# Kernel tuning notes

Hardware: AMD Instinct MI355X
Metric: run time of the kernel (lower is better)

The kernel has to match this reference:

```python
import jax, jax.numpy as jnp
import numpy as np

N = 50000
NEG_SLOPE = 0.2

def gat_conv(x, src, dst, W, a_src, a_dst, bias, heads, out_ch):
    # Linear projection per head: [N, H, C]
    h = (x @ W).reshape(x.shape[0], heads, out_ch)
    # Node-level attention terms alpha_src/alpha_dst: [N, H]
    al_src = jnp.einsum('nhc,hc->nh', h, a_src)
    al_dst = jnp.einsum('nhc,hc->nh', h, a_dst)
    # Edge logits with LeakyReLU: [E, H]
    logits = jax.nn.leaky_relu(al_src[src] + al_dst[dst], NEG_SLOPE)
    # Segment softmax over incoming edges of each dst node
    m = jax.ops.segment_max(logits, dst, num_segments=N)
    e = jnp.exp(logits - m[dst])
    s = jax.ops.segment_sum(e, dst, num_segments=N)
    alpha = e / (s[dst] + 1e-16)                      # [E, H]
    # Weighted message aggregation (scatter-add): [N, H, C]
    out = jax.ops.segment_sum(h[src] * alpha[..., None], dst, num_segments=N)
    return out.reshape(N, heads * out_ch) + bias


def setup_inputs() -> dict:
    key = jax.random.key(0)
    ks = jax.random.split(key, 12)
    in_ch, out_ch = 128, 256
    h1, c1 = 4, out_ch // 8          # conv1: 4 heads x 32
    mid = h1 * c1                    # 128 = out_ch // 2
    E = 1600000
    x = jax.random.normal(ks[0], (N, in_ch), jnp.float32)
    edge_index = jax.random.randint(ks[1], (2, E), 0, N, jnp.int64)
    sc = 0.1
    return {
        'x': x,
        'edge_index': edge_index,
        'W1': jax.random.normal(ks[2], (in_ch, h1 * c1), jnp.float32) * sc,
        'a_src1': jax.random.normal(ks[3], (h1, c1), jnp.float32) * sc,
        'a_dst1': jax.random.normal(ks[4], (h1, c1), jnp.float32) * sc,
        'b1': jnp.zeros((h1 * c1,), jnp.float32),
        'W2': jax.random.normal(ks[5], (mid, out_ch), jnp.float32) * sc,
        'a_src2': jax.random.normal(ks[6], (1, out_ch), jnp.float32) * sc,
        'a_dst2': jax.random.normal(ks[7], (1, out_ch), jnp.float32) * sc,
        'b2': jnp.zeros((out_ch,), jnp.float32),
    }


def reference(x, edge_index, W1, a_src1, a_dst1, b1, W2, a_src2, a_dst2, b2):
    # PyG GATConv adds self-loops by default
    loop = jnp.arange(N, dtype=edge_index.dtype)
    src = jnp.concatenate([edge_index[0], loop])
    dst = jnp.concatenate([edge_index[1], loop])
    h = gat_conv(x, src, dst, W1, a_src1, a_dst1, b1, heads=4, out_ch=32)
    h = jax.nn.relu(h)
    out = gat_conv(h, src, dst, W2, a_src2, a_dst2, b2, heads=1, out_ch=256)
    return out
```

## Files before the change

### kernel.cpp

```cpp
#include <hip/hip_runtime.h>
#include <hip/hip_fp16.h>
#include <math.h>

#define NSLOPE 0.2f

typedef _Float16 half8 __attribute__((ext_vector_type(8)));
typedef float floatx4 __attribute__((ext_vector_type(4)));

__device__ __forceinline__ float lrelu(float t) { return t > 0.f ? t : NSLOPE * t; }

__device__ __forceinline__ void fma8h(float* acc, float w, const uint4& v) {
    const __half2* h2 = reinterpret_cast<const __half2*>(&v);
#pragma unroll
    for (int i = 0; i < 4; ++i) {
        float2 f = __half22float2(h2[i]);
        acc[2 * i]     = fmaf(w, f.x, acc[2 * i]);
        acc[2 * i + 1] = fmaf(w, f.y, acc[2 * i + 1]);
    }
}

#define MAXB 5632
#define BE   8192

__global__ __launch_bounds__(256)
void bucketA_kernel(const int* __restrict__ src, const int* __restrict__ dst,
                    int* __restrict__ bcnt, int E, int Etot, int nb)
{
    __shared__ int hist[512];
    int tid = threadIdx.x;
    for (int i = tid; i < 512; i += 256) hist[i] = 0;
    __syncthreads();
    for (int e = blockIdx.x * 256 + tid; e < Etot; e += gridDim.x * 256) {
        int d = (e < E) ? dst[e] : (e - E);
        atomicAdd(&hist[d >> 7], 1);
    }
    __syncthreads();
    for (int i = tid; i < nb; i += 256) {
        int v = hist[i];
        if (v) atomicAdd(&bcnt[i], v);
    }
}

__global__ __launch_bounds__(512)
void scanBuckets_kernel(const int* __restrict__ bcnt, int* __restrict__ bbase,
                        int* __restrict__ gcur, int nb, int* __restrict__ offs,
                        int N, int total)
{
    __shared__ int tmp[512];
    int tid = threadIdx.x;
    int v = (tid < nb) ? bcnt[tid] : 0;
    tmp[tid] = v;
    __syncthreads();
    for (int off = 1; off < 512; off <<= 1) {
        int t = (tid >= off) ? tmp[tid - off] : 0;
        __syncthreads();
        tmp[tid] += t;
        __syncthreads();
    }
    if (tid < nb) {
        int e = tmp[tid] - v;
        bbase[tid] = e;
        gcur[tid] = e;
    }
    if (tid == 0) offs[N] = total;
}

__global__ __launch_bounds__(256)
void bucketB_kernel(const int* __restrict__ src, const int* __restrict__ dst,
                    int* __restrict__ gcur, unsigned* __restrict__ eout,
                    int E, int Etot, int nb)
{
    __shared__ int hist[512];
    __shared__ int res[512];
    __shared__ int lcur[512];
    int tid = threadIdx.x;
    int e0 = blockIdx.x * BE;
    int e1 = min(e0 + BE, Etot);

    for (int i = tid; i < 512; i += 256) hist[i] = 0;
    __syncthreads();
    for (int e = e0 + tid; e < e1; e += 256) {
        int d = (e < E) ? dst[e] : (e - E);
        atomicAdd(&hist[d >> 7], 1);
    }
    __syncthreads();
    for (int i = tid; i < nb; i += 256) {
        int h = hist[i];
        res[i] = h ? atomicAdd(&gcur[i], h) : 0;
        lcur[i] = 0;
    }
    __syncthreads();
    for (int e = e0 + tid; e < e1; e += 256) {
        int s, d;
        if (e < E) { s = src[e]; d = dst[e]; }
        else       { s = e - E; d = s; }
        int b = d >> 7;
        int p = res[b] + atomicAdd(&lcur[b], 1);
        eout[p] = (unsigned)s | ((unsigned)(d & 127) << 16);
    }
}

__global__ __launch_bounds__(256)
void bucketC_kernel(const unsigned* __restrict__ eout, const int* __restrict__ bbase,
                    const int* __restrict__ bcnt, unsigned short* __restrict__ csr,
                    int* __restrict__ offs, int N)
{
    __shared__ unsigned eb[MAXB];
    __shared__ unsigned short sbuf[MAXB];
    __shared__ int cnt128[128], cur128[128], sc[128];

    int b = blockIdx.x;
    int tid = threadIdx.x;
    int ebase = bbase[b];
    int ecnt = bcnt[b];
    int n0 = b << 7;
    int ncount = min(128, N - n0);

    if (tid < 128) cnt128[tid] = 0;
    for (int i = tid; i < ecnt; i += 256) eb[i] = eout[ebase + i];
    __syncthreads();
    for (int i = tid; i < ecnt; i += 256) atomicAdd(&cnt128[eb[i] >> 16], 1);
    __syncthreads();
    if (tid < 128) sc[tid] = cnt128[tid];
    __syncthreads();
    for (int off = 1; off < 128; off <<= 1) {
        int t = (tid >= off && tid < 128) ? sc[tid - off] : 0;
        __syncthreads();
        if (tid < 128) sc[tid] += t;
        __syncthreads();
    }
    if (tid < 128) {
        int excl = sc[tid] - cnt128[tid];
        cur128[tid] = excl;
        if (tid < ncount) offs[n0 + tid] = ebase + excl;
    }
    __syncthreads();
    for (int i = tid; i < ecnt; i += 256) {
        unsigned v = eb[i];
        int p = atomicAdd(&cur128[v >> 16], 1);
        sbuf[p] = (unsigned short)(v & 0xFFFFu);
    }
    __syncthreads();
    for (int i = tid; i < ecnt; i += 256) csr[ebase + i] = sbuf[i];
}

__global__ __launch_bounds__(256)
void w2sd_kernel(const float* __restrict__ W2, const float* __restrict__ a_src2,
                 const float* __restrict__ a_dst2, float* __restrict__ w2s,
                 float* __restrict__ w2d)
{
    int t = threadIdx.x;
    const float* a = (t < 128) ? a_src2 : a_dst2;
    int k = t & 127;
    float acc = 0.f;
    for (int c = 0; c < 256; c += 4) {
        float4 w = *(const float4*)&W2[(size_t)k * 256 + c];
        float4 av = *(const float4*)&a[c];
        acc = fmaf(w.x, av.x, fmaf(w.y, av.y, fmaf(w.z, av.z, fmaf(w.w, av.w, acc))));
    }
    if (t < 128) w2s[k] = acc; else w2d[k] = acc;
}

__global__ __launch_bounds__(256)
void cast_f2h_kernel(const float* __restrict__ in, __half* __restrict__ out, int n)
{
    int i = (blockIdx.x * 256 + threadIdx.x) * 4;
    if (i >= n) return;
    float4 v = *(const float4*)&in[i];
    __half2 a = __floats2half2_rn(v.x, v.y);
    __half2 b = __floats2half2_rn(v.z, v.w);
    *(uint2*)&out[i] = make_uint2(*(unsigned*)&a, *(unsigned*)&b);
}

__global__ __launch_bounds__(128)
void transposeW_kernel(const float* __restrict__ W, __half* __restrict__ WT, int C)
{
    int c = blockIdx.x;
    int k = threadIdx.x;
    WT[(size_t)c * 128 + k] = __float2half(W[(size_t)k * C + c]);
}

__global__ __launch_bounds__(256)
void gemm1_mfma(const __half* __restrict__ A16, const __half* __restrict__ W1T,
                const float* __restrict__ a_src, const float* __restrict__ a_dst,
                __half* __restrict__ h1, float* __restrict__ al_src,
                float* __restrict__ al_dst, int M)
{
    int wave = threadIdx.x >> 6, lane = threadIdx.x & 63;
    int lr = lane & 15, q = lane >> 4;
    int r0 = blockIdx.x * 32 + (wave >> 1) * 16;
    int wcol = (wave & 1) * 64;

    int arow = min(r0 + lr, M - 1);
    const uint4* Arow = (const uint4*)A16 + (size_t)arow * 16;
    half8 a[4];
#pragma unroll
    for (int kb = 0; kb < 4; ++kb) {
        union { uint4 u; half8 h; } c;
        c.u = Arow[kb * 4 + q];
        a[kb] = c.h;
    }

    floatx4 acc[4];
    const floatx4 zero = {0.f, 0.f, 0.f, 0.f};
#pragma unroll
    for (int ct = 0; ct < 4; ++ct) acc[ct] = zero;

#pragma unroll
    for (int ct = 0; ct < 4; ++ct) {
        const uint4* Brow = (const uint4*)W1T + (size_t)(wcol + ct * 16 + lr) * 16;
#pragma unroll
        for (int kb = 0; kb < 4; ++kb) {
            union { uint4 u; half8 h; } c;
            c.u = Brow[kb * 4 + q];
            acc[ct] = __builtin_amdgcn_mfma_f32_16x16x32_f16(a[kb], c.h, acc[ct], 0, 0, 0);
        }
    }

#pragma unroll
    for (int ct = 0; ct < 4; ++ct) {
        int col = wcol + ct * 16 + lr;
#pragma unroll
        for (int r = 0; r < 4; ++r) {
            int row = r0 + q * 4 + r;
            if (row < M) h1[(size_t)row * 128 + col] = __float2half(acc[ct][r]);
        }
    }

    float as[4], ad[4];
#pragma unroll
    for (int ct = 0; ct < 4; ++ct) {
        int col = wcol + ct * 16 + lr;
        as[ct] = a_src[col];
        ad[ct] = a_dst[col];
    }
    int hb = wcol >> 5;
#pragma unroll
    for (int r = 0; r < 4; ++r) {
        float psA = acc[0][r] * as[0] + acc[1][r] * as[1];
        float psB = acc[2][r] * as[2] + acc[3][r] * as[3];
        float pdA = acc[0][r] * ad[0] + acc[1][r] * ad[1];
        float pdB = acc[2][r] * ad[2] + acc[3][r] * ad[3];
#pragma unroll
        for (int off = 1; off < 16; off <<= 1) {
            psA += __shfl_xor(psA, off); psB += __shfl_xor(psB, off);
            pdA += __shfl_xor(pdA, off); pdB += __shfl_xor(pdB, off);
        }
        if (lr == 0) {
            int row = r0 + q * 4 + r;
            if (row < M) {
                al_src[(size_t)row * 4 + hb]     = psA;
                al_src[(size_t)row * 4 + hb + 1] = psB;
                al_dst[(size_t)row * 4 + hb]     = pdA;
                al_dst[(size_t)row * 4 + hb + 1] = pdB;
            }
        }
    }
}

__global__ __launch_bounds__(256)
void gemm2_mfma(const __half* __restrict__ A16, const __half* __restrict__ W2T,
                const float* __restrict__ bias, float* __restrict__ out, int M)
{
    int wave = threadIdx.x >> 6, lane = threadIdx.x & 63;
    int lr = lane & 15, q = lane >> 4;
    int r0 = blockIdx.x * 16;
    int c0 = wave * 64;

    int arow = min(r0 + lr, M - 1);
    const uint4* Arow = (const uint4*)A16 + (size_t)arow * 16;
    half8 a[4];
#pragma unroll
    for (int kb = 0; kb < 4; ++kb) {
        union { uint4 u; half8 h; } c;
        c.u = Arow[kb * 4 + q];
        a[kb] = c.h;
    }

    floatx4 acc[4];
    const floatx4 zero = {0.f, 0.f, 0.f, 0.f};
#pragma unroll
    for (int ct = 0; ct < 4; ++ct) acc[ct] = zero;

#pragma unroll
    for (int ct = 0; ct < 4; ++ct) {
        const uint4* Brow = (const uint4*)W2T + (size_t)(c0 + ct * 16 + lr) * 16;
#pragma unroll
        for (int kb = 0; kb < 4; ++kb) {
            union { uint4 u; half8 h; } c;
            c.u = Brow[kb * 4 + q];
            acc[ct] = __builtin_amdgcn_mfma_f32_16x16x32_f16(a[kb], c.h, acc[ct], 0, 0, 0);
        }
    }

#pragma unroll
    for (int ct = 0; ct < 4; ++ct) {
        int col = c0 + ct * 16 + lr;
        float b = bias[col];
#pragma unroll
        for (int r = 0; r < 4; ++r) {
            int row = r0 + q * 4 + r;
            if (row < M) out[(size_t)row * 256 + col] = acc[ct][r] + b;
        }
    }
}

__global__ __launch_bounds__(256)
void agg1_kernel(const __half* __restrict__ feat, const unsigned short* __restrict__ csr_src,
                 const int* __restrict__ offs, const float* __restrict__ alS,
                 const float* __restrict__ alD, const float* __restrict__ bias,
                 const float* __restrict__ w2s, const float* __restrict__ w2d,
                 __half* __restrict__ hmid, float* __restrict__ alS2,
                 float* __restrict__ alD2, int N)
{
    int lane = threadIdx.x & 63;
    int n = blockIdx.x * 4 + (threadIdx.x >> 6);
    if (n >= N) return;

    int lc = lane & 15;
    int es = lane >> 4;
    int h = lc >> 2;

    float aD = alD[(size_t)n * 4 + h];
    int beg = offs[n], end = offs[n + 1];

    float acc0[8] = {0,0,0,0,0,0,0,0}, acc1[8] = {0,0,0,0,0,0,0,0};
    float sw0 = 0.f, sw1 = 0.f;
    const uint4* feat16 = (const uint4*)feat;

    int j = beg + es;
    for (; j + 4 < end; j += 8) {
        int s0 = csr_src[j];
        int s1 = csr_src[j + 4];
        float w0 = __expf(lrelu(alS[(size_t)s0 * 4 + h] + aD));
        float w1 = __expf(lrelu(alS[(size_t)s1 * 4 + h] + aD));
        uint4 f0 = feat16[(size_t)s0 * 16 + lc];
        uint4 f1 = feat16[(size_t)s1 * 16 + lc];
        fma8h(acc0, w0, f0); sw0 += w0;
        fma8h(acc1, w1, f1); sw1 += w1;
    }
    if (j < end) {
        int s0 = csr_src[j];
        float w0 = __expf(lrelu(alS[(size_t)s0 * 4 + h] + aD));
        uint4 f0 = feat16[(size_t)s0 * 16 + lc];
        fma8h(acc0, w0, f0); sw0 += w0;
    }

    float sw = sw0 + sw1;
    sw += __shfl_xor(sw, 16); sw += __shfl_xor(sw, 32);
#pragma unroll
    for (int i = 0; i < 8; ++i) {
        acc0[i] += acc1[i];
        acc0[i] += __shfl_xor(acc0[i], 16);
        acc0[i] += __shfl_xor(acc0[i], 32);
    }

    if (lane < 16) {
        float inv = 1.f / (sw + 1e-16f);
        float v[8];
#pragma unroll
        for (int i = 0; i < 8; ++i)
            v[i] = fmaxf(fmaf(acc0[i], inv, bias[lc * 8 + i]), 0.f);
        __half2 p0 = __floats2half2_rn(v[0], v[1]);
        __half2 p1 = __floats2half2_rn(v[2], v[3]);
        __half2 p2 = __floats2half2_rn(v[4], v[5]);
        __half2 p3 = __floats2half2_rn(v[6], v[7]);
        uint4 pk = make_uint4(*(unsigned*)&p0, *(unsigned*)&p1,
                              *(unsigned*)&p2, *(unsigned*)&p3);
        ((uint4*)hmid)[(size_t)n * 16 + lc] = pk;
        float ps = 0.f, pd = 0.f;
#pragma unroll
        for (int i = 0; i < 8; ++i) {
            ps = fmaf(v[i], w2s[lc * 8 + i], ps);
            pd = fmaf(v[i], w2d[lc * 8 + i], pd);
        }
        ps += __shfl_xor(ps, 1); ps += __shfl_xor(ps, 2);
        ps += __shfl_xor(ps, 4); ps += __shfl_xor(ps, 8);
        pd += __shfl_xor(pd, 1); pd += __shfl_xor(pd, 2);
        pd += __shfl_xor(pd, 4); pd += __shfl_xor(pd, 8);
        if (lane == 0) { alS2[n] = ps; alD2[n] = pd; }
    }
}

__global__ __launch_bounds__(256)
void agg2_kernel(const __half* __restrict__ feat, const unsigned short* __restrict__ csr_src,
                 const int* __restrict__ offs, const float* __restrict__ alS,
                 const float* __restrict__ alD, __half* __restrict__ m16, int N)
{
    int lane = threadIdx.x & 63;
    int n = blockIdx.x * 4 + (threadIdx.x >> 6);
    if (n >= N) return;

    int lc = lane & 15;
    int es = lane >> 4;

    float aD = alD[n];
    int beg = offs[n], end = offs[n + 1];

    float acc0[8] = {0,0,0,0,0,0,0,0}, acc1[8] = {0,0,0,0,0,0,0,0};
    float sw0 = 0.f, sw1 = 0.f;
    const uint4* feat16 = (const uint4*)feat;

    int j = beg + es;
    for (; j + 4 < end; j += 8) {
        int s0 = csr_src[j];
        int s1 = csr_src[j + 4];
        float w0 = __expf(lrelu(alS[s0] + aD));
        float w1 = __expf(lrelu(alS[s1] + aD));
        uint4 f0 = feat16[(size_t)s0 * 16 + lc];
        uint4 f1 = feat16[(size_t)s1 * 16 + lc];
        fma8h(acc0, w0, f0); sw0 += w0;
        fma8h(acc1, w1, f1); sw1 += w1;
    }
    if (j < end) {
        int s0 = csr_src[j];
        float w0 = __expf(lrelu(alS[s0] + aD));
        uint4 f0 = feat16[(size_t)s0 * 16 + lc];
        fma8h(acc0, w0, f0); sw0 += w0;
    }

    float sw = sw0 + sw1;
    sw += __shfl_xor(sw, 16); sw += __shfl_xor(sw, 32);
#pragma unroll
    for (int i = 0; i < 8; ++i) {
        acc0[i] += acc1[i];
        acc0[i] += __shfl_xor(acc0[i], 16);
        acc0[i] += __shfl_xor(acc0[i], 32);
    }

    if (lane < 16) {
        float inv = 1.f / (sw + 1e-16f);
        float v[8];
#pragma unroll
        for (int i = 0; i < 8; ++i) v[i] = acc0[i] * inv;
        __half2 p0 = __floats2half2_rn(v[0], v[1]);
        __half2 p1 = __floats2half2_rn(v[2], v[3]);
        __half2 p2 = __floats2half2_rn(v[4], v[5]);
        __half2 p3 = __floats2half2_rn(v[6], v[7]);
        uint4 pk = make_uint4(*(unsigned*)&p0, *(unsigned*)&p1,
                              *(unsigned*)&p2, *(unsigned*)&p3);
        ((uint4*)m16)[(size_t)n * 16 + lc] = pk;
    }
}

extern "C" void kernel_launch(void* const* d_in, const int* in_sizes, int n_in,
                              void* d_out, int out_size, void* d_ws, size_t ws_size,
                              hipStream_t stream)
{
    const float* x      = (const float*)d_in[0];
    const int*   ei     = (const int*)d_in[1];
    const float* W1     = (const float*)d_in[2];
    const float* a_src1 = (const float*)d_in[3];
    const float* a_dst1 = (const float*)d_in[4];
    const float* b1     = (const float*)d_in[5];
    const float* W2     = (const float*)d_in[6];
    const float* a_src2 = (const float*)d_in[7];
    const float* a_dst2 = (const float*)d_in[8];
    const float* b2     = (const float*)d_in[9];

    const int N    = in_sizes[0] / 128;
    const int E    = in_sizes[1] / 2;
    const int Etot = E + N;
    const int* src = ei;
    const int* dst = ei + E;
    const int nb   = (N + 127) >> 7;

    char* ws = (char*)d_ws;
    size_t off = 0;
    auto carve = [&](size_t bytes) -> void* {
        void* p = ws + off;
        off += (bytes + 255) & ~(size_t)255;
        return p;
    };
    __half*  x16  = (__half*)carve((size_t)N * 128 * 2);
    __half*  h1   = (__half*)carve((size_t)N * 128 * 2);
    __half*  hmid = (__half*)carve((size_t)N * 128 * 2);
    __half*  m16  = (__half*)carve((size_t)N * 128 * 2);
    __half*  W1T  = (__half*)carve(128 * 128 * 2);
    __half*  W2T  = (__half*)carve(256 * 128 * 2);
    float*   alS1 = (float*)carve((size_t)N * 4 * 4);
    float*   alD1 = (float*)carve((size_t)N * 4 * 4);
    float*   alS2 = (float*)carve((size_t)N * 4);
    float*   alD2 = (float*)carve((size_t)N * 4);
    float*   w2s  = (float*)carve(128 * 4);
    float*   w2d  = (float*)carve(128 * 4);
    int*     offs = (int*)carve((size_t)(N + 1) * 4);
    int*     bcnt = (int*)carve(512 * 4);
    int*     bbas = (int*)carve(512 * 4);
    int*     gcur = (int*)carve(512 * 4);
    unsigned* eout = (unsigned*)carve((size_t)Etot * 4);
    unsigned short* csr = (unsigned short*)carve((size_t)Etot * 2);
    (void)ws_size; (void)n_in; (void)out_size;

    const int TB = 256;
    const int agrid = (N + 3) / 4;
    const int g1grid = (N + 31) / 32;
    const int g2grid = (N + 15) / 16;
    const int nx = N * 128;

    hipMemsetAsync(bcnt, 0, 512 * 4, stream);

    bucketA_kernel<<<512, TB, 0, stream>>>(src, dst, bcnt, E, Etot, nb);
    scanBuckets_kernel<<<1, 512, 0, stream>>>(bcnt, bbas, gcur, nb, offs, N, Etot);
    bucketB_kernel<<<(Etot + BE - 1) / BE, TB, 0, stream>>>(src, dst, gcur, eout, E, Etot, nb);
    bucketC_kernel<<<nb, TB, 0, stream>>>(eout, bbas, bcnt, csr, offs, N);

    cast_f2h_kernel<<<(nx / 4 + TB - 1) / TB, TB, 0, stream>>>(x, x16, nx);
    transposeW_kernel<<<128, 128, 0, stream>>>(W1, W1T, 128);
    transposeW_kernel<<<256, 128, 0, stream>>>(W2, W2T, 256);
    w2sd_kernel<<<1, 256, 0, stream>>>(W2, a_src2, a_dst2, w2s, w2d);

    gemm1_mfma<<<g1grid, 256, 0, stream>>>(x16, W1T, a_src1, a_dst1, h1, alS1, alD1, N);
    agg1_kernel<<<agrid, 256, 0, stream>>>(h1, csr, offs, alS1, alD1, b1,
                                           w2s, w2d, hmid, alS2, alD2, N);

    agg2_kernel<<<agrid, 256, 0, stream>>>(hmid, csr, offs, alS2, alD2, m16, N);
    gemm2_mfma<<<g2grid, 256, 0, stream>>>(m16, W2T, b2, (float*)d_out, N);
}
```

Before: 330.8 us.

## Merge independent prep kernels and co-schedule CSR bucketing with first GEMM

Folds bucket histogramming, the x cast, both weight transposes and the w2s/w2d projection into one block-partitioned prep kernel. It also merges the CSR bucketC pass with gemm1 into one combo kernel, so these independent stages share a launch and overlap on the GPU. This cuts launch count and idle tails between small kernels. In exchange, the combo kernel carries the large shared-memory footprint of the bucketing path into the GEMM blocks, which may lower their occupancy. The aggregation kernels also switch to byte-offset addressing for feature gathers, a minor address-arithmetic tweak.

```diff
diff --git a/kernel.cpp b/kernel.cpp
--- a/kernel.cpp
+++ b/kernel.cpp
@@ -23,21 +23,67 @@
 #define BE   8192
 
 __global__ __launch_bounds__(256)
-void bucketA_kernel(const int* __restrict__ src, const int* __restrict__ dst,
-                    int* __restrict__ bcnt, int E, int Etot, int nb)
+void prep_kernel(const int* __restrict__ dst, int* __restrict__ bcnt,
+                 const float* __restrict__ x, __half* __restrict__ x16, int nx,
+                 const float* __restrict__ W1, __half* __restrict__ W1T,
+                 const float* __restrict__ W2, __half* __restrict__ W2T,
+                 const float* __restrict__ a_src2, const float* __restrict__ a_dst2,
+                 float* __restrict__ w2s, float* __restrict__ w2d,
+                 int E, int Etot, int nb, int nbA, int ncast, int nt1, int nt2)
 {
     __shared__ int hist[512];
+    int bid = blockIdx.x;
     int tid = threadIdx.x;
-    for (int i = tid; i < 512; i += 256) hist[i] = 0;
-    __syncthreads();
-    for (int e = blockIdx.x * 256 + tid; e < Etot; e += gridDim.x * 256) {
-        int d = (e < E) ? dst[e] : (e - E);
-        atomicAdd(&hist[d >> 7], 1);
-    }
-    __syncthreads();
-    for (int i = tid; i < nb; i += 256) {
-        int v = hist[i];
-        if (v) atomicAdd(&bcnt[i], v);
+
+    if (bid < nbA) {
+        for (int i = tid; i < 512; i += 256) hist[i] = 0;
+        __syncthreads();
+        for (int e = bid * 256 + tid; e < Etot; e += nbA * 256) {
+            int d = (e < E) ? dst[e] : (e - E);
+            atomicAdd(&hist[d >> 7], 1);
+        }
+        __syncthreads();
+        for (int i = tid; i < nb; i += 256) {
+            int v = hist[i];
+            if (v) atomicAdd(&bcnt[i], v);
+        }
+        return;
+    }
+    bid -= nbA;
+    if (bid < ncast) {
+        int i = (bid * 256 + tid) * 4;
+        if (i < nx) {
+            float4 v = *(const float4*)&x[i];
+            __half2 a = __floats2half2_rn(v.x, v.y);
+            __half2 b = __floats2half2_rn(v.z, v.w);
+            *(uint2*)&x16[i] = make_uint2(*(unsigned*)&a, *(unsigned*)&b);
+        }
+        return;
+    }
+    bid -= ncast;
+    if (bid < nt1) {
+        int idx = bid * 256 + tid;
+        int c = idx >> 7, k = idx & 127;
+        W1T[(size_t)c * 128 + k] = __float2half(W1[(size_t)k * 128 + c]);
+        return;
+    }
+    bid -= nt1;
+    if (bid < nt2) {
+        int idx = bid * 256 + tid;
+        int c = idx >> 7, k = idx & 127;
+        W2T[(size_t)c * 128 + k] = __float2half(W2[(size_t)k * 256 + c]);
+        return;
+    }
+    {
+        const float* a = (tid < 128) ? a_src2 : a_dst2;
+        int k = tid & 127;
+        float acc = 0.f;
+        for (int c = 0; c < 256; c += 4) {
+            float4 w = *(const float4*)&W2[(size_t)k * 256 + c];
+            float4 av = *(const float4*)&a[c];
+            acc = fmaf(w.x, av.x, fmaf(w.y, av.y, fmaf(w.z, av.z, fmaf(w.w, av.w, acc))));
+        }
+        if (tid < 128) w2s[k] = acc; else w2d[k] = acc;
     }
 }
 
@@ -101,94 +147,60 @@
 }
 
 __global__ __launch_bounds__(256)
-void bucketC_kernel(const unsigned* __restrict__ eout, const int* __restrict__ bbase,
-                    const int* __restrict__ bcnt, unsigned short* __restrict__ csr,
-                    int* __restrict__ offs, int N)
+void combo_kernel(const unsigned* __restrict__ eout, const int* __restrict__ bbase,
+                  const int* __restrict__ bcnt, unsigned short* __restrict__ csr,
+                  int* __restrict__ offs, int N, int nb,
+                  const __half* __restrict__ A16, const __half* __restrict__ W1T,
+                  const float* __restrict__ a_src, const float* __restrict__ a_dst,
+                  __half* __restrict__ h1, float* __restrict__ al_src,
+                  float* __restrict__ al_dst)
 {
     __shared__ unsigned eb[MAXB];
     __shared__ unsigned short sbuf[MAXB];
     __shared__ int cnt128[128], cur128[128], sc[128];
 
-    int b = blockIdx.x;
     int tid = threadIdx.x;
-    int ebase = bbase[b];
-    int ecnt = bcnt[b];
-    int n0 = b << 7;
-    int ncount = min(128, N - n0);
-
-    if (tid < 128) cnt128[tid] = 0;
-    for (int i = tid; i < ecnt; i += 256) eb[i] = eout[ebase + i];
-    __syncthreads();
-    for (int i = tid; i < ecnt; i += 256) atomicAdd(&cnt128[eb[i] >> 16], 1);
-    __syncthreads();
-    if (tid < 128) sc[tid] = cnt128[tid];
-    __syncthreads();
-    for (int off = 1; off < 128; off <<= 1) {
-        int t = (tid >= off && tid < 128) ? sc[tid - off] : 0;
-        __syncthreads();
-        if (tid < 128) sc[tid] += t;
-        __syncthreads();
-    }
-    if (tid < 128) {
-        int excl = sc[tid] - cnt128[tid];
-        cur128[tid] = excl;
-        if (tid < ncount) offs[n0 + tid] = ebase + excl;
-    }
-    __syncthreads();
-    for (int i = tid; i < ecnt; i += 256) {
-        unsigned v = eb[i];
-        int p = atomicAdd(&cur128[v >> 16], 1);
-        sbuf[p] = (unsigned short)(v & 0xFFFFu);
-    }
-    __syncthreads();
-    for (int i = tid; i < ecnt; i += 256) csr[ebase + i] = sbuf[i];
-}
-
-__global__ __launch_bounds__(256)
-void w2sd_kernel(const float* __restrict__ W2, const float* __restrict__ a_src2,
-                 const float* __restrict__ a_dst2, float* __restrict__ w2s,
-                 float* __restrict__ w2d)
-{
-    int t = threadIdx.x;
-    const float* a = (t < 128) ? a_src2 : a_dst2;
-    int k = t & 127;
-    float acc = 0.f;
-    for (int c = 0; c < 256; c += 4) {
-        float4 w = *(const float4*)&W2[(size_t)k * 256 + c];
-        float4 av = *(const float4*)&a[c];
-        acc = fmaf(w.x, av.x, fmaf(w.y, av.y, fmaf(w.z, av.z, fmaf(w.w, av.w, acc))));
-    }
-    if (t < 128) w2s[k] = acc; else w2d[k] = acc;
-}
-
-__global__ __launch_bounds__(256)
-void cast_f2h_kernel(const float* __restrict__ in, __half* __restrict__ out, int n)
-{
-    int i = (blockIdx.x * 256 + threadIdx.x) * 4;
-    if (i >= n) return;
-    float4 v = *(const float4*)&in[i];
-    __half2 a = __floats2half2_rn(v.x, v.y);
-    __half2 b = __floats2half2_rn(v.z, v.w);
-    *(uint2*)&out[i] = make_uint2(*(unsigned*)&a, *(unsigned*)&b);
-}
-
-__global__ __launch_bounds__(128)
-void transposeW_kernel(const float* __restrict__ W, __half* __restrict__ WT, int C)
-{
-    int c = blockIdx.x;
-    int k = threadIdx.x;
-    WT[(size_t)c * 128 + k] = __float2half(W[(size_t)k * C + c]);
-}
-
-__global__ __launch_bounds__(256)
-void gemm1_mfma(const __half* __restrict__ A16, const __half* __restrict__ W1T,
-                const float* __restrict__ a_src, const float* __restrict__ a_dst,
-                __half* __restrict__ h1, float* __restrict__ al_src,
-                float* __restrict__ al_dst, int M)
-{
-    int wave = threadIdx.x >> 6, lane = threadIdx.x & 63;
+    if ((int)blockIdx.x < nb) {
+        int b = blockIdx.x;
+        int ebase = bbase[b];
+        int ecnt = bcnt[b];
+        int n0 = b << 7;
+        int ncount = min(128, N - n0);
+
+        if (tid < 128) cnt128[tid] = 0;
+        for (int i = tid; i < ecnt; i += 256) eb[i] = eout[ebase + i];
+        __syncthreads();
+        for (int i = tid; i < ecnt; i += 256) atomicAdd(&cnt128[eb[i] >> 16], 1);
+        __syncthreads();
+        if (tid < 128) sc[tid] = cnt128[tid];
+        __syncthreads();
+        for (int off = 1; off < 128; off <<= 1) {
+            int t = (tid >= off && tid < 128) ? sc[tid - off] : 0;
+            __syncthreads();
+            if (tid < 128) sc[tid] += t;
+            __syncthreads();
+        }
+        if (tid < 128) {
+            int excl = sc[tid] - cnt128[tid];
+            cur128[tid] = excl;
+            if (tid < ncount) offs[n0 + tid] = ebase + excl;
+        }
+        __syncthreads();
+        for (int i = tid; i < ecnt; i += 256) {
+            unsigned v = eb[i];
+            int p = atomicAdd(&cur128[v >> 16], 1);
+            sbuf[p] = (unsigned short)(v & 0xFFFFu);
+        }
+        __syncthreads();
+        for (int i = tid; i < ecnt; i += 256) csr[ebase + i] = sbuf[i];
+        return;
+    }
+
+    int gb = blockIdx.x - nb;
+    int M = N;
+    int wave = tid >> 6, lane = tid & 63;
     int lr = lane & 15, q = lane >> 4;
-    int r0 = blockIdx.x * 32 + (wave >> 1) * 16;
+    int r0 = gb * 32 + (wave >> 1) * 16;
     int wcol = (wave & 1) * 64;
 
     int arow = min(r0 + lr, M - 1);
@@ -326,7 +338,7 @@
 
     float acc0[8] = {0,0,0,0,0,0,0,0}, acc1[8] = {0,0,0,0,0,0,0,0};
     float sw0 = 0.f, sw1 = 0.f;
-    const uint4* feat16 = (const uint4*)feat;
+    const char* fbase = (const char*)feat + lc * 16;
 
     int j = beg + es;
     for (; j + 4 < end; j += 8) {
@@ -334,15 +346,15 @@
         int s1 = csr_src[j + 4];
         float w0 = __expf(lrelu(alS[(size_t)s0 * 4 + h] + aD));
         float w1 = __expf(lrelu(alS[(size_t)s1 * 4 + h] + aD));
-        uint4 f0 = feat16[(size_t)s0 * 16 + lc];
-        uint4 f1 = feat16[(size_t)s1 * 16 + lc];
+        uint4 f0 = *(const uint4*)(fbase + (size_t)s0 * 256);
+        uint4 f1 = *(const uint4*)(fbase + (size_t)s1 * 256);
         fma8h(acc0, w0, f0); sw0 += w0;
         fma8h(acc1, w1, f1); sw1 += w1;
     }
     if (j < end) {
         int s0 = csr_src[j];
         float w0 = __expf(lrelu(alS[(size_t)s0 * 4 + h] + aD));
-        uint4 f0 = feat16[(size_t)s0 * 16 + lc];
+        uint4 f0 = *(const uint4*)(fbase + (size_t)s0 * 256);
         fma8h(acc0, w0, f0); sw0 += w0;
     }
 
@@ -399,7 +411,7 @@
 
     float acc0[8] = {0,0,0,0,0,0,0,0}, acc1[8] = {0,0,0,0,0,0,0,0};
     float sw0 = 0.f, sw1 = 0.f;
-    const uint4* feat16 = (const uint4*)feat;
+    const char* fbase = (const char*)feat + lc * 16;
 
     int j = beg + es;
     for (; j + 4 < end; j += 8) {
@@ -407,15 +419,15 @@
         int s1 = csr_src[j + 4];
         float w0 = __expf(lrelu(alS[s0] + aD));
         float w1 = __expf(lrelu(alS[s1] + aD));
-        uint4 f0 = feat16[(size_t)s0 * 16 + lc];
-        uint4 f1 = feat16[(size_t)s1 * 16 + lc];
+        uint4 f0 = *(const uint4*)(fbase + (size_t)s0 * 256);
+        uint4 f1 = *(const uint4*)(fbase + (size_t)s1 * 256);
         fma8h(acc0, w0, f0); sw0 += w0;
         fma8h(acc1, w1, f1); sw1 += w1;
     }
     if (j < end) {
         int s0 = csr_src[j];
         float w0 = __expf(lrelu(alS[s0] + aD));
-        uint4 f0 = feat16[(size_t)s0 * 16 + lc];
+        uint4 f0 = *(const uint4*)(fbase + (size_t)s0 * 256);
         fma8h(acc0, w0, f0); sw0 += w0;
     }
 
@@ -498,22 +510,23 @@
     const int g2grid = (N + 15) / 16;
     const int nx = N * 128;
 
+    const int nbA   = 512;
+    const int ncast = (nx / 4 + TB - 1) / TB;
+    const int nt1   = (128 * 128 + TB - 1) / TB;
+    const int nt2   = (256 * 128 + TB - 1) / TB;
+    const int nprep = nbA + ncast + nt1 + nt2 + 1;
+
     hipMemsetAsync(bcnt, 0, 512 * 4, stream);
 
-    bucketA_kernel<<<512, TB, 0, stream>>>(src, dst, bcnt, E, Etot, nb);
+    prep_kernel<<<nprep, TB, 0, stream>>>(dst, bcnt, x, x16, nx, W1, W1T, W2, W2T,
+                                          a_src2, a_dst2, w2s, w2d,
+                                          E, Etot, nb, nbA, ncast, nt1, nt2);
     scanBuckets_kernel<<<1, 512, 0, stream>>>(bcnt, bbas, gcur, nb, offs, N, Etot);
     bucketB_kernel<<<(Etot + BE - 1) / BE, TB, 0, stream>>>(src, dst, gcur, eout, E, Etot, nb);
-    bucketC_kernel<<<nb, TB, 0, stream>>>(eout, bbas, bcnt, csr, offs, N);
-
-    cast_f2h_kernel<<<(nx / 4 + TB - 1) / TB, TB, 0, stream>>>(x, x16, nx);
-    transposeW_kernel<<<128, 128, 0, stream>>>(W1, W1T, 128);
-    transposeW_kernel<<<256, 128, 0, stream>>>(W2, W2T, 256);
-    w2sd_kernel<<<1, 256, 0, stream>>>(W2, a_src2, a_dst2, w2s, w2d);
-
-    gemm1_mfma<<<g1grid, 256, 0, stream>>>(x16, W1T, a_src1, a_dst1, h1, alS1, alD1, N);
-    agg1_kernel<<<agrid, 256, 0, stream>>>(h1, csr, offs, alS1, alD1, b1,
-                                           w2s, w2d, hmid, alS2, alD2, N);
-
-    agg2_kernel<<<agrid, 256, 0, stream>>>(hmid, csr, offs, alS2, alD2, m16, N);
-    gemm2_mfma<<<g2grid, 256, 0, stream>>>(m16, W2T, b2, (float*)d_out, N);
-}
+    combo_kernel<<<nb + g1grid, TB, 0, stream>>>(eout, bbas, bcnt, csr, offs, N, nb,
+                                                 x16, W1T, a_src1, a_dst1, h1, alS1, alD1);
+    agg1_kernel<<<agrid, TB, 0, stream>>>(h1, csr, offs, alS1, alD1, b1,
+                                          w2s, w2d, hmid, alS2, alD2, N);
+    agg2_kernel<<<agrid, TB, 0, stream>>>(hmid, csr, offs, alS2, alD2, m16, N);
+    gemm2_mfma<<<g2grid, TB, 0, stream>>>(m16, W2T, b2, (float*)d_out, N);
+}
```

Result: faster. 305.9 us (-7.5%).
